# Performance work log

Hardware: AMD Instinct MI355X
Metric: run time of the kernel (lower is better)

Reference implementation:

```python
import jax, jax.numpy as jnp
import numpy as np

DIM = 192
HEADS = 8
HEAD_DIM = DIM // HEADS
SCALE = HEAD_DIM ** (-0.5)
H = W = 64
EPS = 1e-12  # F.normalize default eps


def setup_inputs() -> dict:
    key = jax.random.key(0)
    k1, k2, k3, k4 = jax.random.split(key, 4)
    x = jax.random.normal(k1, (1, DIM, H, W), jnp.float32)
    w_qkv = jax.random.normal(k2, (3 * DIM, DIM), jnp.float32) * 0.05   # 1x1 conv dim->3*dim
    w_dw = jax.random.normal(k3, (3 * DIM, 1, 3, 3), jnp.float32) * 0.05  # depthwise 3x3, groups=3*dim
    w_proj = jax.random.normal(k4, (DIM, DIM), jnp.float32) * 0.05      # 1x1 conv dim->dim
    return {"x": x, "w_qkv": w_qkv, "w_dw": w_dw, "w_proj": w_proj}


def reference(x, w_qkv, w_dw, w_proj):
    B, C, h, w = x.shape
    n = h * w
    # 1x1 conv (no bias) == channel matmul
    qkv = jnp.einsum('oc,bchw->bohw', w_qkv, x)
    # depthwise 3x3 conv, padding=1
    qkv = jax.lax.conv_general_dilated(
        qkv, w_dw, window_strides=(1, 1), padding='SAME',
        dimension_numbers=('NCHW', 'OIHW', 'NCHW'),
        feature_group_count=3 * C)
    q, k, v = jnp.split(qkv, 3, axis=1)

    def to_heads(t):  # [B,C,h,w] -> [B,heads,HW,head_dim]
        return t.reshape(B, HEADS, HEAD_DIM, n).transpose(0, 1, 3, 2)

    q, k, v = to_heads(q), to_heads(k), to_heads(v)
    # L2-normalize along head_dim (F.normalize semantics)
    q = q / jnp.maximum(jnp.linalg.norm(q, axis=-1, keepdims=True), EPS)
    k = k / jnp.maximum(jnp.linalg.norm(k, axis=-1, keepdims=True), EPS)
    attn = jax.nn.softmax(jnp.einsum('bhnd,bhmd->bhnm', q, k) * SCALE, axis=-1)
    out = jnp.einsum('bhnm,bhmd->bhnd', attn, v)  # [B,heads,HW,head_dim]
    out = out.transpose(0, 1, 3, 2).reshape(B, C, h, w)
    return jnp.einsum('oc,bchw->bohw', w_proj, out)
```

## Files before the change

kernel.cpp:

```cpp
#include <hip/hip_runtime.h>

typedef unsigned short u16;
typedef unsigned int u32;
typedef short bf16x8 __attribute__((ext_vector_type(8)));
typedef float f32x4 __attribute__((ext_vector_type(4)));

__device__ __forceinline__ u16 f2bf(float f) {
  union { float f; unsigned int u; } a; a.f = f;
  unsigned int r = a.u + 0x7FFFu + ((a.u >> 16) & 1u);
  return (u16)(r >> 16);
}
__device__ __forceinline__ float bf2f(u16 b) {
  return __uint_as_float(((u32)b) << 16);
}

__global__ __launch_bounds__(256) void prep(const float* __restrict__ X,
                                            const float* __restrict__ W,
                                            const float* __restrict__ Wp,
                                            u16* __restrict__ Xt,
                                            u16* __restrict__ Wb,
                                            u16* __restrict__ Wpb) {
  int b = blockIdx.x;
  int t = threadIdx.x;
  if (b < 128) {
    __shared__ float Xl[192 * 33];
    int p0 = b << 5;
    int px = t & 31, cs = t >> 5;
    #pragma unroll
    for (int i = 0; i < 24; ++i) {
      int c = cs * 24 + i;
      Xl[c * 33 + px] = X[(size_t)c * 4096 + p0 + px];
    }
    __syncthreads();
    int pxo = t >> 3, j0 = (t & 7) * 12;
    u32* Xt32 = (u32*)Xt;
    #pragma unroll
    for (int jj = 0; jj < 12; ++jj) {
      int j = j0 + jj;
      u32 v = ((u32)f2bf(Xl[(2 * j + 1) * 33 + pxo]) << 16) |
              f2bf(Xl[(2 * j) * 33 + pxo]);
      Xt32[(size_t)(p0 + pxo) * 96 + j] = v;
    }
  } else if (b < 182) {
    int idx = (b - 128) * 2048 + t * 8;
    #pragma unroll
    for (int i = 0; i < 8; ++i) Wb[idx + i] = f2bf(W[idx + i]);
  } else {
    int idx = (b - 182) * 2048 + t * 8;
    #pragma unroll
    for (int i = 0; i < 8; ++i) Wpb[idx + i] = f2bf(Wp[idx + i]);
  }
}

template <bool B16>
__global__ __launch_bounds__(256) void mqkv(const u16* __restrict__ Wb,
                                            const u16* __restrict__ Xt,
                                            void* __restrict__ Yv) {
  __shared__ u16 Sl[4][32 * 32];
  int tid = threadIdx.x;
  int wave = tid >> 6, lane = tid & 63;
  int lo = lane & 15, hi = lane >> 4;
  int m0 = blockIdx.y << 5;
  int n0 = (blockIdx.x << 7) + (wave << 5);
  f32x4 zz = {0.f, 0.f, 0.f, 0.f};
  f32x4 acc00 = zz, acc01 = zz, acc10 = zz, acc11 = zz;
  #pragma unroll
  for (int k0 = 0; k0 < 192; k0 += 32) {
    bf16x8 a0 = *(const bf16x8*)(Wb + (size_t)(m0 + lo) * 192 + k0 + hi * 8);
    bf16x8 a1 = *(const bf16x8*)(Wb + (size_t)(m0 + 16 + lo) * 192 + k0 + hi * 8);
    bf16x8 b0 = *(const bf16x8*)(Xt + (size_t)(n0 + lo) * 192 + k0 + hi * 8);
    bf16x8 b1 = *(const bf16x8*)(Xt + (size_t)(n0 + 16 + lo) * 192 + k0 + hi * 8);
    acc00 = __builtin_amdgcn_mfma_f32_16x16x32_bf16(a0, b0, acc00, 0, 0, 0);
    acc01 = __builtin_amdgcn_mfma_f32_16x16x32_bf16(a0, b1, acc01, 0, 0, 0);
    acc10 = __builtin_amdgcn_mfma_f32_16x16x32_bf16(a1, b0, acc10, 0, 0, 0);
    acc11 = __builtin_amdgcn_mfma_f32_16x16x32_bf16(a1, b1, acc11, 0, 0, 0);
  }
  if (B16) {
    u16* S = Sl[wave];
    #pragma unroll
    for (int r = 0; r < 4; ++r) {
      S[(hi * 4 + r) * 32 + lo] = f2bf(acc00[r]);
      S[(hi * 4 + r) * 32 + 16 + lo] = f2bf(acc01[r]);
      S[(16 + hi * 4 + r) * 32 + lo] = f2bf(acc10[r]);
      S[(16 + hi * 4 + r) * 32 + 16 + lo] = f2bf(acc11[r]);
    }
    const u32* S32 = (const u32*)S;
    u32* Y32 = (u32*)Yv;
    #pragma unroll
    for (int i = lane; i < 512; i += 64) {
      int row = i >> 4, j = i & 15;
      Y32[(size_t)(m0 + row) * 2048 + (n0 >> 1) + j] = S32[row * 16 + j];
    }
  } else {
    float* Y = (float*)Yv;
    #pragma unroll
    for (int r = 0; r < 4; ++r) {
      Y[(size_t)(m0 + hi * 4 + r) * 4096 + n0 + lo] = acc00[r];
      Y[(size_t)(m0 + hi * 4 + r) * 4096 + n0 + 16 + lo] = acc01[r];
      Y[(size_t)(m0 + 16 + hi * 4 + r) * 4096 + n0 + lo] = acc10[r];
      Y[(size_t)(m0 + 16 + hi * 4 + r) * 4096 + n0 + 16 + lo] = acc11[r];
    }
  }
}

__global__ __launch_bounds__(256) void dwconv3(const u16* __restrict__ in,
                                               const float* __restrict__ w,
                                               u16* __restrict__ out) {
  int idx = blockIdx.x * 256 + threadIdx.x;
  int c = idx >> 12;
  int p = idx & 4095;
  int y = p >> 6, x = p & 63;
  const float* wc = w + c * 9;
  const u16* ic = in + (size_t)c * 4096;
  float s = 0.f;
  #pragma unroll
  for (int i = 0; i < 3; ++i) {
    int yy = y + i - 1;
    if ((unsigned)yy >= 64u) continue;
    #pragma unroll
    for (int j = 0; j < 3; ++j) {
      int xx = x + j - 1;
      if ((unsigned)xx >= 64u) continue;
      s = fmaf(wc[i * 3 + j], bf2f(ic[yy * 64 + xx]), s);
    }
  }
  out[idx] = f2bf(s);
}

__global__ __launch_bounds__(256) void nvpack(const u16* __restrict__ qkv,
                                              u32* __restrict__ Qh32,
                                              u32* __restrict__ Kh32,
                                              u32* __restrict__ Vt32) {
  __shared__ u32 Ql[128 * 17];
  __shared__ u32 Kl[128 * 17];
  __shared__ u16 Vl[32 * 128];
  int t = threadIdx.x;
  int bid = blockIdx.x;
  int h = bid >> 5;
  int p0 = (bid & 31) << 7;
  u32* Vl32 = (u32*)Vl;
  const float QSC = 0.20412414523193154f * 1.4426950408889634f;
  if (t < 128) {
    int p = p0 + t;
    float qv[24], kv[24];
    float sq = 0.f, sk = 0.f;
    #pragma unroll
    for (int d = 0; d < 24; ++d) {
      qv[d] = bf2f(qkv[(size_t)(h * 24 + d) * 4096 + p]);
      sq = fmaf(qv[d], qv[d], sq);
    }
    #pragma unroll
    for (int d = 0; d < 24; ++d) {
      kv[d] = bf2f(qkv[(size_t)(192 + h * 24 + d) * 4096 + p]);
      sk = fmaf(kv[d], kv[d], sk);
    }
    float iq = QSC / fmaxf(sqrtf(sq), 1e-12f);
    float ik = 1.0f / fmaxf(sqrtf(sk), 1e-12f);
    u32* qrow = Ql + t * 17;
    u32* krow = Kl + t * 17;
    #pragma unroll
    for (int j = 0; j < 12; ++j) {
      qrow[j] = ((u32)f2bf(qv[2 * j + 1] * iq) << 16) | f2bf(qv[2 * j] * iq);
      krow[j] = ((u32)f2bf(kv[2 * j + 1] * ik) << 16) | f2bf(kv[2 * j] * ik);
    }
    #pragma unroll
    for (int j = 12; j < 16; ++j) { qrow[j] = 0; krow[j] = 0; }
  } else {
    int tl = t - 128;
    int p = p0 + tl;
    int kp = (tl & ~63) | (tl & 32) | (((tl >> 2) & 3) << 3) |
             (((tl >> 4) & 1) << 2) | (tl & 3);
    #pragma unroll
    for (int d = 0; d < 24; ++d)
      Vl[d * 128 + kp] = qkv[(size_t)(384 + h * 24 + d) * 4096 + p];
    Vl[24 * 128 + kp] = 0x3F80;
  }
  for (int i = t; i < 7 * 64; i += 256) Vl32[25 * 64 + i] = 0;
  __syncthreads();
  size_t base = ((size_t)(h << 12) + p0) * 16;
  for (int i = t; i < 2048; i += 256) {
    u32 li = (i >> 4) * 17 + (i & 15);
    Qh32[base + i] = Ql[li];
    Kh32[base + i] = Kl[li];
  }
  for (int i = t; i < 2048; i += 256) {
    int d = i >> 6, c = i & 63;
    Vt32[(((size_t)(h * 32 + d)) << 11) + (p0 >> 1) + c] = Vl32[d * 64 + c];
  }
}

__device__ __forceinline__ bf16x8 pexp(f32x4 a, f32x4 b) {
  union { u32 u[4]; bf16x8 v; } x;
  u32 a0 = __float_as_uint(__builtin_amdgcn_exp2f(a[0]));
  u32 a1 = __float_as_uint(__builtin_amdgcn_exp2f(a[1]));
  u32 a2 = __float_as_uint(__builtin_amdgcn_exp2f(a[2]));
  u32 a3 = __float_as_uint(__builtin_amdgcn_exp2f(a[3]));
  u32 b0 = __float_as_uint(__builtin_amdgcn_exp2f(b[0]));
  u32 b1 = __float_as_uint(__builtin_amdgcn_exp2f(b[1]));
  u32 b2 = __float_as_uint(__builtin_amdgcn_exp2f(b[2]));
  u32 b3 = __float_as_uint(__builtin_amdgcn_exp2f(b[3]));
  x.u[0] = __builtin_amdgcn_perm(a1, a0, 0x07060302u);
  x.u[1] = __builtin_amdgcn_perm(a3, a2, 0x07060302u);
  x.u[2] = __builtin_amdgcn_perm(b1, b0, 0x07060302u);
  x.u[3] = __builtin_amdgcn_perm(b3, b2, 0x07060302u);
  return x.v;
}

__global__ __launch_bounds__(512, 3) void attn(const u16* __restrict__ Qh,
                                               const u16* __restrict__ Kh,
                                               const u16* __restrict__ Vt,
                                               u16* __restrict__ Pt) {
  __shared__ float Sf[8 * 64 * 28];
  __shared__ u16 Pb[64 * 24];
  int tid = threadIdx.x;
  int wave = tid >> 6, lane = tid & 63;
  int lo = lane & 15, hi = lane >> 4;
  int b = blockIdx.x;
  int head = b & 7;
  int q0 = (b >> 3) << 7;

  const u16* Kb = Kh + ((size_t)head << 17);
  const u16* Vb = Vt + ((size_t)head << 17);

  size_t qrow = (size_t)(head << 12) + q0 + lo;
  bf16x8 qf[8];
  #pragma unroll
  for (int f = 0; f < 8; ++f)
    qf[f] = *(const bf16x8*)(Qh + ((qrow + f * 16) << 5) + hi * 8);

  f32x4 zz = {0.f, 0.f, 0.f, 0.f};
  f32x4 oA[8], oB[8];
  #pragma unroll
  for (int f = 0; f < 8; ++f) { oA[f] = zz; oB[f] = zz; }

  int kbase = wave << 9;

  for (int it = 0; it < 8; ++it) {
    int k0 = kbase + it * 64;
    bf16x8 kf[4], vf[4];
    #pragma unroll
    for (int j = 0; j < 4; ++j)
      kf[j] = *(const bf16x8*)(Kb + (((size_t)(k0 + j * 16 + lo)) << 5) + hi * 8);
    vf[0] = *(const bf16x8*)(Vb + (((size_t)(lo)) << 12) + k0 + hi * 8);
    vf[1] = *(const bf16x8*)(Vb + (((size_t)(16 + lo)) << 12) + k0 + hi * 8);
    vf[2] = *(const bf16x8*)(Vb + (((size_t)(lo)) << 12) + k0 + 32 + hi * 8);
    vf[3] = *(const bf16x8*)(Vb + (((size_t)(16 + lo)) << 12) + k0 + 32 + hi * 8);
    #pragma unroll
    for (int f = 0; f < 8; ++f) {
      f32x4 t0 = __builtin_amdgcn_mfma_f32_16x16x32_bf16(kf[0], qf[f], zz, 0, 0, 0);
      f32x4 t1 = __builtin_amdgcn_mfma_f32_16x16x32_bf16(kf[1], qf[f], zz, 0, 0, 0);
      f32x4 t2 = __builtin_amdgcn_mfma_f32_16x16x32_bf16(kf[2], qf[f], zz, 0, 0, 0);
      f32x4 t3 = __builtin_amdgcn_mfma_f32_16x16x32_bf16(kf[3], qf[f], zz, 0, 0, 0);
      bf16x8 a0 = pexp(t0, t1);
      bf16x8 a1 = pexp(t2, t3);
      oA[f] = __builtin_amdgcn_mfma_f32_16x16x32_bf16(a0, vf[0], oA[f], 0, 0, 0);
      oB[f] = __builtin_amdgcn_mfma_f32_16x16x32_bf16(a0, vf[1], oB[f], 0, 0, 0);
      oA[f] = __builtin_amdgcn_mfma_f32_16x16x32_bf16(a1, vf[2], oA[f], 0, 0, 0);
      oB[f] = __builtin_amdgcn_mfma_f32_16x16x32_bf16(a1, vf[3], oB[f], 0, 0, 0);
    }
  }

  const u32* Pb32 = (const u32*)Pb;
  u32* Pt32 = (u32*)Pt;
  #pragma unroll
  for (int pass = 0; pass < 2; ++pass) {
    int sb = wave * (64 * 28);
    #pragma unroll
    for (int fl = 0; fl < 4; ++fl) {
      int f = pass * 4 + fl;
      #pragma unroll
      for (int r = 0; r < 4; ++r) {
        int row = fl * 16 + hi * 4 + r;
        Sf[sb + row * 28 + lo] = oA[f][r];
        if (lo < 8) Sf[sb + row * 28 + 16 + lo] = oB[f][r];
        if (lo == 8) Sf[sb + row * 28 + 24] = oB[f][r];
      }
    }
    __syncthreads();
    int q = tid & 63;
    int d0 = tid >> 6;
    int base0 = q * 28;
    const int SS = 64 * 28;
    float den = 0.f;
    #pragma unroll
    for (int s = 0; s < 8; ++s) den += Sf[base0 + s * SS + 24];
    float inv = 1.0f / den;
    #pragma unroll
    for (int dp = 0; dp < 3; ++dp) {
      int dd = dp * 8 + d0;
      float v = 0.f;
      #pragma unroll
      for (int s = 0; s < 8; ++s) v += Sf[base0 + s * SS + dd];
      Pb[q * 24 + dd] = f2bf(v * inv);
    }
    __syncthreads();
    for (int i = tid; i < 768; i += 512) {
      int qq = i / 12, j = i - qq * 12;
      Pt32[(size_t)(q0 + pass * 64 + qq) * 96 + head * 12 + j] = Pb32[qq * 12 + j];
    }
  }
}

extern "C" void kernel_launch(void* const* d_in, const int* in_sizes, int n_in,
                              void* d_out, int out_size, void* d_ws, size_t ws_size,
                              hipStream_t stream) {
  const float* x      = (const float*)d_in[0];
  const float* w_qkv  = (const float*)d_in[1];
  const float* w_dw   = (const float*)d_in[2];
  const float* w_proj = (const float*)d_in[3];
  float* out = (float*)d_out;

  char* ws = (char*)d_ws;
  u16*   qkv    = (u16*)  (ws);
  u16*   qkvd   = (u16*)  (ws + 4718592);
  u16*   Qh     = (u16*)  (ws + 18874368);
  u16*   Kh     = (u16*)  (ws + 20971520);
  u16*   Vt     = (u16*)  (ws + 23068672);
  u16*   Xt     = (u16*)  (ws + 25165824);
  u16*   Wb     = (u16*)  (ws + 26738688);
  u16*   Wpb    = (u16*)  (ws + 26959872);
  u16*   Pt     = (u16*)  (ws + 13107200);

  prep<<<dim3(200), 256, 0, stream>>>(x, w_qkv, w_proj, Xt, Wb, Wpb);
  mqkv<true><<<dim3(32, 18), 256, 0, stream>>>(Wb, Xt, qkv);
  dwconv3<<<dim3(9216), 256, 0, stream>>>(qkv, w_dw, qkvd);
  nvpack<<<dim3(256), 256, 0, stream>>>(qkvd, (u32*)Qh, (u32*)Kh, (u32*)Vt);
  attn<<<dim3(256), 512, 0, stream>>>(Qh, Kh, Vt, Pt);
  mqkv<false><<<dim3(32, 6), 256, 0, stream>>>(Wpb, Pt, out);
}
```

Before: 125.1 us.

## Switch attention MFMA from 16x16x32 to 32x32x16 with permlane32 swap

Rewrites the attention inner loop to use 32x32x16 bf16 MFMAs for both QK^T and PV, and converts the score layout to the PV A-operand with v_permlane32_swap instead of pre-permuting V columns in the prep kernel. The prep kernel now writes V in natural order. s_setprio hints are added around the MFMA groups, and the shared staging buffer is padded to 29 floats per row for the new output layout. Occupancy drops from 3 to 2 blocks per CU because the larger accumulator tiles raise register pressure.

New measurement: 121.6 us. 1.03x faster.

```diff
diff --git a/kernel.cpp b/kernel.cpp
--- a/kernel.cpp
+++ b/kernel.cpp
@@ -4,6 +4,7 @@
 typedef unsigned int u32;
 typedef short bf16x8 __attribute__((ext_vector_type(8)));
 typedef float f32x4 __attribute__((ext_vector_type(4)));
+typedef float f32x16 __attribute__((ext_vector_type(16)));
 
 __device__ __forceinline__ u16 f2bf(float f) {
   union { float f; unsigned int u; } a; a.f = f;
@@ -168,12 +169,10 @@
   } else {
     int tl = t - 128;
     int p = p0 + tl;
-    int kp = (tl & ~63) | (tl & 32) | (((tl >> 2) & 3) << 3) |
-             (((tl >> 4) & 1) << 2) | (tl & 3);
     #pragma unroll
     for (int d = 0; d < 24; ++d)
-      Vl[d * 128 + kp] = qkv[(size_t)(384 + h * 24 + d) * 4096 + p];
-    Vl[24 * 128 + kp] = 0x3F80;
+      Vl[d * 128 + tl] = qkv[(size_t)(384 + h * 24 + d) * 4096 + p];
+    Vl[24 * 128 + tl] = 0x3F80;
   }
   for (int i = t; i < 7 * 64; i += 256) Vl32[25 * 64 + i] = 0;
   __syncthreads();
@@ -189,32 +188,27 @@
   }
 }
 
-__device__ __forceinline__ bf16x8 pexp(f32x4 a, f32x4 b) {
+__device__ __forceinline__ void swp32(u32& a, u32& b) {
+  asm("v_permlane32_swap_b32 %0, %1" : "+v"(a), "+v"(b));
+}
+
+__device__ __forceinline__ bf16x8 mkfrag(u32 a, u32 b, u32 c, u32 d) {
   union { u32 u[4]; bf16x8 v; } x;
-  u32 a0 = __float_as_uint(__builtin_amdgcn_exp2f(a[0]));
-  u32 a1 = __float_as_uint(__builtin_amdgcn_exp2f(a[1]));
-  u32 a2 = __float_as_uint(__builtin_amdgcn_exp2f(a[2]));
-  u32 a3 = __float_as_uint(__builtin_amdgcn_exp2f(a[3]));
-  u32 b0 = __float_as_uint(__builtin_amdgcn_exp2f(b[0]));
-  u32 b1 = __float_as_uint(__builtin_amdgcn_exp2f(b[1]));
-  u32 b2 = __float_as_uint(__builtin_amdgcn_exp2f(b[2]));
-  u32 b3 = __float_as_uint(__builtin_amdgcn_exp2f(b[3]));
-  x.u[0] = __builtin_amdgcn_perm(a1, a0, 0x07060302u);
-  x.u[1] = __builtin_amdgcn_perm(a3, a2, 0x07060302u);
-  x.u[2] = __builtin_amdgcn_perm(b1, b0, 0x07060302u);
-  x.u[3] = __builtin_amdgcn_perm(b3, b2, 0x07060302u);
+  x.u[0] = a; x.u[1] = b; x.u[2] = c; x.u[3] = d;
   return x.v;
 }
 
-__global__ __launch_bounds__(512, 3) void attn(const u16* __restrict__ Qh,
+#define MFMA32(A, B, C) __builtin_amdgcn_mfma_f32_32x32x16_bf16(A, B, C, 0, 0, 0)
+
+__global__ __launch_bounds__(512, 2) void attn(const u16* __restrict__ Qh,
                                                const u16* __restrict__ Kh,
                                                const u16* __restrict__ Vt,
                                                u16* __restrict__ Pt) {
-  __shared__ float Sf[8 * 64 * 28];
+  __shared__ float Sf[8 * 64 * 29];
   __shared__ u16 Pb[64 * 24];
   int tid = threadIdx.x;
   int wave = tid >> 6, lane = tid & 63;
-  int lo = lane & 15, hi = lane >> 4;
+  int l31 = lane & 31, h5 = lane >> 5;
   int b = blockIdx.x;
   int head = b & 7;
   int q0 = (b >> 3) << 7;
@@ -222,41 +216,61 @@
   const u16* Kb = Kh + ((size_t)head << 17);
   const u16* Vb = Vt + ((size_t)head << 17);
 
-  size_t qrow = (size_t)(head << 12) + q0 + lo;
-  bf16x8 qf[8];
+  size_t qbase = ((size_t)head << 12) + q0;
+  bf16x8 qf[4][2];
   #pragma unroll
-  for (int f = 0; f < 8; ++f)
-    qf[f] = *(const bf16x8*)(Qh + ((qrow + f * 16) << 5) + hi * 8);
-
-  f32x4 zz = {0.f, 0.f, 0.f, 0.f};
-  f32x4 oA[8], oB[8];
-  #pragma unroll
-  for (int f = 0; f < 8; ++f) { oA[f] = zz; oB[f] = zz; }
+  for (int qb = 0; qb < 4; ++qb)
+    #pragma unroll
+    for (int c = 0; c < 2; ++c)
+      qf[qb][c] = *(const bf16x8*)(Qh + ((qbase + qb * 32 + l31) << 5) +
+                                   c * 16 + h5 * 8);
+
+  f32x16 oC[4] = {};
 
   int kbase = wave << 9;
 
   for (int it = 0; it < 8; ++it) {
     int k0 = kbase + it * 64;
-    bf16x8 kf[4], vf[4];
-    #pragma unroll
-    for (int j = 0; j < 4; ++j)
-      kf[j] = *(const bf16x8*)(Kb + (((size_t)(k0 + j * 16 + lo)) << 5) + hi * 8);
-    vf[0] = *(const bf16x8*)(Vb + (((size_t)(lo)) << 12) + k0 + hi * 8);
-    vf[1] = *(const bf16x8*)(Vb + (((size_t)(16 + lo)) << 12) + k0 + hi * 8);
-    vf[2] = *(const bf16x8*)(Vb + (((size_t)(lo)) << 12) + k0 + 32 + hi * 8);
-    vf[3] = *(const bf16x8*)(Vb + (((size_t)(16 + lo)) << 12) + k0 + 32 + hi * 8);
-    #pragma unroll
-    for (int f = 0; f < 8; ++f) {
-      f32x4 t0 = __builtin_amdgcn_mfma_f32_16x16x32_bf16(kf[0], qf[f], zz, 0, 0, 0);
-      f32x4 t1 = __builtin_amdgcn_mfma_f32_16x16x32_bf16(kf[1], qf[f], zz, 0, 0, 0);
-      f32x4 t2 = __builtin_amdgcn_mfma_f32_16x16x32_bf16(kf[2], qf[f], zz, 0, 0, 0);
-      f32x4 t3 = __builtin_amdgcn_mfma_f32_16x16x32_bf16(kf[3], qf[f], zz, 0, 0, 0);
-      bf16x8 a0 = pexp(t0, t1);
-      bf16x8 a1 = pexp(t2, t3);
-      oA[f] = __builtin_amdgcn_mfma_f32_16x16x32_bf16(a0, vf[0], oA[f], 0, 0, 0);
-      oB[f] = __builtin_amdgcn_mfma_f32_16x16x32_bf16(a0, vf[1], oB[f], 0, 0, 0);
-      oA[f] = __builtin_amdgcn_mfma_f32_16x16x32_bf16(a1, vf[2], oA[f], 0, 0, 0);
-      oB[f] = __builtin_amdgcn_mfma_f32_16x16x32_bf16(a1, vf[3], oB[f], 0, 0, 0);
+    bf16x8 kf[2][2], vf[4];
+    #pragma unroll
+    for (int g = 0; g < 2; ++g)
+      #pragma unroll
+      for (int c = 0; c < 2; ++c)
+        kf[g][c] = *(const bf16x8*)(Kb + (((size_t)(k0 + g * 32 + l31)) << 5) +
+                                    c * 16 + h5 * 8);
+    #pragma unroll
+    for (int c4 = 0; c4 < 4; ++c4)
+      vf[c4] = *(const bf16x8*)(Vb + (((size_t)l31) << 12) + k0 + c4 * 16 +
+                                h5 * 8);
+    #pragma unroll
+    for (int qb = 0; qb < 4; ++qb) {
+      __builtin_amdgcn_s_setprio(1);
+      f32x16 s0{}, s1{};
+      s0 = MFMA32(kf[0][0], qf[qb][0], s0);
+      s0 = MFMA32(kf[0][1], qf[qb][1], s0);
+      s1 = MFMA32(kf[1][0], qf[qb][0], s1);
+      s1 = MFMA32(kf[1][1], qf[qb][1], s1);
+      __builtin_amdgcn_s_setprio(0);
+      u32 w[16];
+      #pragma unroll
+      for (int r = 0; r < 8; ++r) {
+        u32 e0 = __float_as_uint(__builtin_amdgcn_exp2f(s0[2 * r]));
+        u32 e1 = __float_as_uint(__builtin_amdgcn_exp2f(s0[2 * r + 1]));
+        w[r] = __builtin_amdgcn_perm(e1, e0, 0x07060302u);
+        u32 e2 = __float_as_uint(__builtin_amdgcn_exp2f(s1[2 * r]));
+        u32 e3 = __float_as_uint(__builtin_amdgcn_exp2f(s1[2 * r + 1]));
+        w[8 + r] = __builtin_amdgcn_perm(e3, e2, 0x07060302u);
+      }
+      swp32(w[0], w[2]);   swp32(w[1], w[3]);
+      swp32(w[4], w[6]);   swp32(w[5], w[7]);
+      swp32(w[8], w[10]);  swp32(w[9], w[11]);
+      swp32(w[12], w[14]); swp32(w[13], w[15]);
+      __builtin_amdgcn_s_setprio(1);
+      oC[qb] = MFMA32(mkfrag(w[0], w[1], w[2], w[3]), vf[0], oC[qb]);
+      oC[qb] = MFMA32(mkfrag(w[4], w[5], w[6], w[7]), vf[1], oC[qb]);
+      oC[qb] = MFMA32(mkfrag(w[8], w[9], w[10], w[11]), vf[2], oC[qb]);
+      oC[qb] = MFMA32(mkfrag(w[12], w[13], w[14], w[15]), vf[3], oC[qb]);
+      __builtin_amdgcn_s_setprio(0);
     }
   }
 
@@ -264,23 +278,21 @@
   u32* Pt32 = (u32*)Pt;
   #pragma unroll
   for (int pass = 0; pass < 2; ++pass) {
-    int sb = wave * (64 * 28);
-    #pragma unroll
-    for (int fl = 0; fl < 4; ++fl) {
-      int f = pass * 4 + fl;
+    int sb = wave * (64 * 29);
+    #pragma unroll
+    for (int qq = 0; qq < 2; ++qq) {
+      int qb = pass * 2 + qq;
       #pragma unroll
-      for (int r = 0; r < 4; ++r) {
-        int row = fl * 16 + hi * 4 + r;
-        Sf[sb + row * 28 + lo] = oA[f][r];
-        if (lo < 8) Sf[sb + row * 28 + 16 + lo] = oB[f][r];
-        if (lo == 8) Sf[sb + row * 28 + 24] = oB[f][r];
+      for (int r = 0; r < 16; ++r) {
+        int row = qq * 32 + (r & 3) + 8 * (r >> 2) + 4 * h5;
+        if (l31 < 25) Sf[sb + row * 29 + l31] = oC[qb][r];
       }
     }
     __syncthreads();
     int q = tid & 63;
     int d0 = tid >> 6;
-    int base0 = q * 28;
-    const int SS = 64 * 28;
+    int base0 = q * 29;
+    const int SS = 64 * 29;
     float den = 0.f;
     #pragma unroll
     for (int s = 0; s < 8; ++s) den += Sf[base0 + s * SS + 24];
```
